# Performance work log

Hardware: AMD Instinct MI355X
Metric: run time of the kernel (lower is better)

The kernel has to match this reference:

```python
import jax, jax.numpy as jnp
import numpy as np

B = 65536
HID = 128
OUT = 10


def setup_inputs() -> dict:
    key = jax.random.key(0)
    ks = jax.random.split(key, 6)
    x = jax.random.normal(ks[0], (B, 784), dtype=jnp.float32)
    conv_w = jax.random.normal(ks[1], (3, 3), dtype=jnp.float32)
    # torch Linear(676,128): weight [128,676], bias [128]
    w1 = jax.random.normal(ks[2], (HID, 26 * 26), dtype=jnp.float32) * (1.0 / np.sqrt(26 * 26))
    b1 = jax.random.normal(ks[3], (HID,), dtype=jnp.float32) * 0.01
    w2 = jax.random.normal(ks[4], (OUT, HID), dtype=jnp.float32) * (1.0 / np.sqrt(HID))
    b2 = jax.random.normal(ks[5], (OUT,), dtype=jnp.float32) * 0.01
    return {"x": x, "conv_w": conv_w, "w1": w1, "b1": b1, "w2": w2, "b2": b2}


def reference(x, conv_w, w1, b1, w2, b2):
    b = x.shape[0]
    img = x.reshape(b, 1, 28, 28)                      # NCHW, single channel
    kern = conv_w.reshape(1, 1, 3, 3)                  # OIHW
    # valid 3x3 cross-correlation (matches the elementwise-multiply-and-sum loop)
    conv = jax.lax.conv_general_dilated(
        img, kern, window_strides=(1, 1), padding="VALID",
        dimension_numbers=("NCHW", "OIHW", "NCHW"))   # [B,1,26,26]
    feat = conv.reshape(b, 26 * 26)
    h = jax.nn.relu(feat @ w1.T + b1)                  # [B,128]
    return h @ w2.T + b2                               # [B,10]
```

## Files before the change

### kernel.cpp

```cpp
#include <hip/hip_runtime.h>
#include <hip/hip_bf16.h>

#define BATCH  65536
#define KREAL  784
#define BK     64
#define NCHUNK 13
#define KPAD   (NCHUNK*BK)
#define HID    128
#define NOUT   10
#define BM     128
#define NTHR   512

using f32x4  = __attribute__((ext_vector_type(4))) float;
using short8 = __attribute__((ext_vector_type(8))) short;
using f4     = __attribute__((ext_vector_type(4))) float;

__device__ inline short f2b(float f) {
    union { __hip_bfloat16 h; short s; } u;
    u.h = __float2bfloat16(f);
    return u.s;
}

#define GLDS16(gp, lp) \
    __builtin_amdgcn_global_load_lds((const __attribute__((address_space(1))) void*)(gp), \
                                     (__attribute__((address_space(3))) void*)(lp), 16, 0, 0)

__global__ void prep_kernel(const float* __restrict__ conv_w,
                            const float* __restrict__ w1,
                            const float* __restrict__ w2,
                            unsigned short* __restrict__ weff_sw,
                            unsigned short* __restrict__ w2p)
{
    const int NW = NCHUNK * HID * BK;
    int idx = blockIdx.x * 256 + threadIdx.x;
    if (idx < NW) {
        int ic  = idx >> 13;
        int rem = idx & 8191;
        int r   = rem >> 6;
        int cc  = rem & 63;
        int g   = (cc >> 3) ^ (r & 7);
        int k   = ic * BK + g * 8 + (cc & 7);
        float acc = 0.f;
        if (k < KREAL) {
            int rr = k / 28, c = k - rr * 28;
            #pragma unroll
            for (int di = 0; di < 3; ++di) {
                int i = rr - di;
                if (i >= 0 && i < 26) {
                    #pragma unroll
                    for (int dj = 0; dj < 3; ++dj) {
                        int j = c - dj;
                        if (j >= 0 && j < 26)
                            acc = fmaf(w1[r * 676 + i * 26 + j], conv_w[di * 3 + dj], acc);
                    }
                }
            }
        }
        weff_sw[idx] = (unsigned short)f2b(acc);
    } else {
        int k = idx - NW;
        if (k < 16 * HID) {
            int o = k >> 7, c = k & 127;
            w2p[k] = (unsigned short)f2b((o < NOUT) ? w2[o * HID + c] : 0.f);
        }
    }
}

__global__ __launch_bounds__(NTHR, 4)
void fused_mlp_kernel(const float* __restrict__ x,
                      const float* __restrict__ b1,
                      const float* __restrict__ b2,
                      const unsigned short* __restrict__ weff_sw,
                      const unsigned short* __restrict__ w2p,
                      float* __restrict__ out)
{
    __shared__ __align__(16) unsigned short smem[16384];
    unsigned short* ldsA = smem;
    unsigned short* ldsB = smem + 8192;
    unsigned short* ldsH = smem;

    const int tid  = threadIdx.x;
    const int wv   = tid >> 6;
    const int lane = tid & 63;
    const int lo   = lane & 15;
    const int hi   = lane >> 4;
    const int row0 = blockIdx.x * BM;
    const int wr0  = wv * 16;

    f32x4 acc[8];
    #pragma unroll
    for (int t = 0; t < 8; ++t) acc[t] = (f32x4){0.f, 0.f, 0.f, 0.f};

    const int rA  = tid >> 2;
    const int qA  = tid & 3;
    const int swA = rA & 7;
    const float* xrow = x + (long)(row0 + rA) * KREAL;
    const f4 fz = {0.f, 0.f, 0.f, 0.f};

    for (int ic = 0; ic < NCHUNK; ++ic) {
        const int kbase = ic * BK;
        __syncthreads();

        {
            const char* src = (const char*)(weff_sw + ic * (HID * BK));
            int o0 = wv * 1024 + lane * 16;
            GLDS16(src + o0,        (char*)ldsB + wv * 1024);
            GLDS16(src + o0 + 8192, (char*)ldsB + wv * 1024 + 8192);
        }
        {
            f4 v[4];
            #pragma unroll
            for (int m = 0; m < 4; ++m) {
                int col = kbase + qA * 16 + m * 4;
                v[m] = (col < KREAL) ? *(const f4*)(xrow + col) : fz;
            }
            short8 c0, c1;
            #pragma unroll
            for (int e = 0; e < 4; ++e) {
                c0[e]     = f2b(v[0][e]);
                c0[4 + e] = f2b(v[1][e]);
                c1[e]     = f2b(v[2][e]);
                c1[4 + e] = f2b(v[3][e]);
            }
            *(short8*)&ldsA[rA * BK + (((2 * qA)     ^ swA) << 3)] = c0;
            *(short8*)&ldsA[rA * BK + (((2 * qA + 1) ^ swA) << 3)] = c1;
        }
        __syncthreads();

        #pragma unroll
        for (int kk = 0; kk < 2; ++kk) {
            const int ra = wr0 + lo;
            const int gA = kk * 4 + hi;
            short8 afrag = *(const short8*)&ldsA[ra * BK + ((gA ^ (ra & 7)) << 3)];
            #pragma unroll
            for (int t = 0; t < 8; ++t) {
                const int ob = t * 16 + lo;
                short8 bfrag = *(const short8*)&ldsB[ob * BK + ((gA ^ (ob & 7)) << 3)];
                acc[t] = __builtin_amdgcn_mfma_f32_16x16x32_bf16(afrag, bfrag, acc[t], 0, 0, 0);
            }
        }
    }

    __syncthreads();

    #pragma unroll
    for (int t = 0; t < 8; ++t) {
        float bias = b1[t * 16 + lo];
        #pragma unroll
        for (int j = 0; j < 4; ++j) {
            float hv = acc[t][j] + bias;
            hv = hv > 0.f ? hv : 0.f;
            int rloc = wr0 + hi * 4 + j;
            int col  = t * 16 + lo;
            int g    = col >> 3, e = col & 7;
            ldsH[rloc * HID + ((g ^ (rloc & 7)) << 3) + e] = (unsigned short)f2b(hv);
        }
    }

    f32x4 acc2 = (f32x4){0.f, 0.f, 0.f, 0.f};
    #pragma unroll
    for (int kk = 0; kk < 4; ++kk) {
        int r = wr0 + lo;
        int g = kk * 4 + hi;
        short8 ha = *(const short8*)&ldsH[r * HID + ((g ^ (r & 7)) << 3)];
        short8 wb = *(const short8*)(w2p + lo * HID + kk * 32 + hi * 8);
        acc2 = __builtin_amdgcn_mfma_f32_16x16x32_bf16(ha, wb, acc2, 0, 0, 0);
    }
    if (lo < NOUT) {
        float bb = b2[lo];
        #pragma unroll
        for (int j = 0; j < 4; ++j) {
            int grow = row0 + wr0 + hi * 4 + j;
            out[grow * NOUT + lo] = acc2[j] + bb;
        }
    }
}

extern "C" void kernel_launch(void* const* d_in, const int* in_sizes, int n_in,
                              void* d_out, int out_size, void* d_ws, size_t ws_size,
                              hipStream_t stream)
{
    const float* x      = (const float*)d_in[0];
    const float* conv_w = (const float*)d_in[1];
    const float* w1     = (const float*)d_in[2];
    const float* b1     = (const float*)d_in[3];
    const float* w2     = (const float*)d_in[4];
    const float* b2     = (const float*)d_in[5];
    float* out = (float*)d_out;

    unsigned short* weff_sw = (unsigned short*)d_ws;
    unsigned short* w2p     = weff_sw + NCHUNK * HID * BK;

    const int prep_total = NCHUNK * HID * BK + 16 * HID;
    prep_kernel<<<(prep_total + 255) / 256, 256, 0, stream>>>(conv_w, w1, w2, weff_sw, w2p);
    fused_mlp_kernel<<<BATCH / BM, NTHR, 0, stream>>>(x, b1, b2, weff_sw, w2p, out);
}
```

Measured before the change: 46.02 us.

## Load A fragments straight to registers and double-buffer weight chunks in LDS

Each wave now loads its own 16 rows of x straight into registers, already in the MFMA fragment layout, so A no longer goes through LDS. The next chunk of A is prefetched into a second register set. The weight tile is double-buffered in LDS: the next chunk is staged while the current one is consumed, and this drops one barrier per iteration. The goal is to hide global-load latency in a kernel bound by memory bandwidth. The cost is higher register pressure, and whether the asynchronous LDS loads are properly waited on before the barrier is a correctness risk.

After: 46.83 us. About the same (+1.8%).

```diff
diff --git a/kernel.cpp b/kernel.cpp
--- a/kernel.cpp
+++ b/kernel.cpp
@@ -75,9 +75,9 @@
                       float* __restrict__ out)
 {
     __shared__ __align__(16) unsigned short smem[16384];
-    unsigned short* ldsA = smem;
-    unsigned short* ldsB = smem + 8192;
-    unsigned short* ldsH = smem;
+    unsigned short* bufB0 = smem;
+    unsigned short* bufB1 = smem + 8192;
+    unsigned short* ldsH  = smem;
 
     const int tid  = threadIdx.x;
     const int wv   = tid >> 6;
@@ -91,52 +91,52 @@
     #pragma unroll
     for (int t = 0; t < 8; ++t) acc[t] = (f32x4){0.f, 0.f, 0.f, 0.f};
 
-    const int rA  = tid >> 2;
-    const int qA  = tid & 3;
-    const int swA = rA & 7;
-    const float* xrow = x + (long)(row0 + rA) * KREAL;
     const f4 fz = {0.f, 0.f, 0.f, 0.f};
+    const float* arow = x + (long)(row0 + wr0 + lo) * KREAL;
 
+    auto loadA = [&](int kbase, f4* v) {
+        #pragma unroll
+        for (int m = 0; m < 4; ++m) {
+            int col = kbase + (m >> 1) * 32 + hi * 8 + (m & 1) * 4;
+            v[m] = (col < KREAL) ? *(const f4*)(arow + col) : fz;
+        }
+    };
+    auto stageB = [&](int ic, unsigned short* dst) {
+        const char* src = (const char*)(weff_sw + ic * (HID * BK));
+        int o0 = wv * 1024 + lane * 16;
+        GLDS16(src + o0,        (char*)dst + wv * 1024);
+        GLDS16(src + o0 + 8192, (char*)dst + wv * 1024 + 8192);
+    };
+
+    f4 av[2][4];
+    loadA(0, av[0]);
+    stageB(0, bufB0);
+
+    #pragma unroll
     for (int ic = 0; ic < NCHUNK; ++ic) {
-        const int kbase = ic * BK;
         __syncthreads();
-
-        {
-            const char* src = (const char*)(weff_sw + ic * (HID * BK));
-            int o0 = wv * 1024 + lane * 16;
-            GLDS16(src + o0,        (char*)ldsB + wv * 1024);
-            GLDS16(src + o0 + 8192, (char*)ldsB + wv * 1024 + 8192);
+        const unsigned short* Bc = (ic & 1) ? bufB1 : bufB0;
+        unsigned short*       Bn = (ic & 1) ? bufB0 : bufB1;
+        if (ic + 1 < NCHUNK) {
+            stageB(ic + 1, Bn);
+            loadA((ic + 1) * BK, av[(ic + 1) & 1]);
         }
-        {
-            f4 v[4];
-            #pragma unroll
-            for (int m = 0; m < 4; ++m) {
-                int col = kbase + qA * 16 + m * 4;
-                v[m] = (col < KREAL) ? *(const f4*)(xrow + col) : fz;
-            }
-            short8 c0, c1;
+        short8 af[2];
+        #pragma unroll
+        for (int kk = 0; kk < 2; ++kk)
             #pragma unroll
             for (int e = 0; e < 4; ++e) {
-                c0[e]     = f2b(v[0][e]);
-                c0[4 + e] = f2b(v[1][e]);
-                c1[e]     = f2b(v[2][e]);
-                c1[4 + e] = f2b(v[3][e]);
+                af[kk][e]     = f2b(av[ic & 1][kk * 2][e]);
+                af[kk][4 + e] = f2b(av[ic & 1][kk * 2 + 1][e]);
             }
-            *(short8*)&ldsA[rA * BK + (((2 * qA)     ^ swA) << 3)] = c0;
-            *(short8*)&ldsA[rA * BK + (((2 * qA + 1) ^ swA) << 3)] = c1;
-        }
-        __syncthreads();
-
         #pragma unroll
         for (int kk = 0; kk < 2; ++kk) {
-            const int ra = wr0 + lo;
             const int gA = kk * 4 + hi;
-            short8 afrag = *(const short8*)&ldsA[ra * BK + ((gA ^ (ra & 7)) << 3)];
             #pragma unroll
             for (int t = 0; t < 8; ++t) {
                 const int ob = t * 16 + lo;
-                short8 bfrag = *(const short8*)&ldsB[ob * BK + ((gA ^ (ob & 7)) << 3)];
-                acc[t] = __builtin_amdgcn_mfma_f32_16x16x32_bf16(afrag, bfrag, acc[t], 0, 0, 0);
+                short8 bfrag = *(const short8*)&Bc[ob * BK + ((gA ^ (ob & 7)) << 3)];
+                acc[t] = __builtin_amdgcn_mfma_f32_16x16x32_bf16(af[kk], bfrag, acc[t], 0, 0, 0);
             }
         }
     }
```
